# Kernel optimization log

Measured on AMD Instinct MI355X. Metric: run time of the kernel, lower is better.

Reference implementation:

```python
import jax, jax.numpy as jnp
import numpy as np
import math

B = 4096
D = 768
HID = 256
C_OLD = 100
C_NEW = 100
NUM_CLASSES = 200
EPSILON = 0.05
TAU = 0.1
EPS = 1e-8
NEG_INF = -1e9


def _l2_normalize(x):
    # matches F.normalize(p=2, dim=1, eps=1e-12)
    n = jnp.linalg.norm(x, axis=1, keepdims=True)
    return x / jnp.maximum(n, 1e-12)


def setup_inputs() -> dict:
    key = jax.random.key(0)
    k1, k2, k3, k4, k5, k6, k7 = jax.random.split(key, 7)
    z_u = jax.random.normal(k1, (B, D), dtype=jnp.float32)
    logits = jax.random.normal(k2, (B, NUM_CLASSES), dtype=jnp.float32)
    old_class_indices = jnp.arange(C_OLD, dtype=jnp.int64 if jax.config.jax_enable_x64 else jnp.int32)
    new_class_indices = jnp.arange(C_OLD, C_OLD + C_NEW, dtype=old_class_indices.dtype)
    base_features = jax.random.normal(k3, (B, D), dtype=jnp.float32)
    s = 1.0 / math.sqrt(D)
    f1_w = jax.random.uniform(k4, (HID, D), dtype=jnp.float32, minval=-s, maxval=s)
    f1_b = jax.random.uniform(k5, (HID,), dtype=jnp.float32, minval=-s, maxval=s)
    f2_w = jax.random.uniform(k6, (HID, D), dtype=jnp.float32, minval=-s, maxval=s)
    f2_b = jax.random.uniform(k7, (HID,), dtype=jnp.float32, minval=-s, maxval=s)
    return {"z_u": z_u, "logits": logits, "old_class_indices": old_class_indices,
            "new_class_indices": new_class_indices, "base_features": base_features,
            "f1_w": f1_w, "f1_b": f1_b, "f2_w": f2_w, "f2_b": f2_b}


def reference(z_u, logits, old_class_indices, new_class_indices, base_features,
              f1_w, f1_b, f2_w, f2_b):
    num_old = old_class_indices.shape[0]
    active = jnp.concatenate([old_class_indices, new_class_indices])

    # ---- soft entropy regularization ----
    probs = jax.nn.softmax(logits[:, active], axis=1)   # (B, C_old+C_new)
    mean_probs = probs.mean(axis=0)
    p_old = mean_probs[:num_old].sum()
    p_new = mean_probs[num_old:].sum()
    loss_inter = (p_old * jnp.log(p_old + EPS) + p_new * jnp.log(p_new + EPS)
                  + math.log(2.0))
    p_old_in = mean_probs[:num_old] / (p_old + EPS)
    loss_old_in = jnp.sum(p_old_in * jnp.log(p_old_in + EPS)) + math.log(num_old)
    p_new_in = mean_probs[num_old:] / (p_new + EPS)
    num_new = new_class_indices.shape[0]
    if num_new > 1:
        loss_new_in = jnp.sum(p_new_in * jnp.log(p_new_in + EPS)) + math.log(num_new)
    else:
        loss_new_in = jnp.float32(0.0)
    loss_entropy = loss_inter + loss_old_in + loss_new_in

    # ---- neighborhood mask from frozen base features ----
    base_norm = _l2_normalize(base_features)
    base_sim = base_norm @ base_norm.T                  # (B, B)
    eye = jnp.eye(base_sim.shape[0], dtype=bool)
    mask = (base_sim > EPSILON) & ~eye                  # (B, B) bool

    # ---- contrastive similarities ----
    z_norm = _l2_normalize(z_u)
    sim = z_norm @ z_norm.T                             # (B, B)

    f1_z = z_u @ f1_w.T + f1_b                          # (B, HID)
    f2_z = z_u @ f2_w.T + f2_b
    attn_logits = jnp.where(mask, f1_z @ f2_z.T, NEG_INF)
    w_ik = jax.nn.softmax(attn_logits, axis=1) * mask.astype(sim.dtype)

    exp_sim = jnp.where(eye, 0.0, jnp.exp(sim / TAU))
    denom = exp_sim.sum(axis=1, keepdims=True)
    log_prob = sim / TAU - jnp.log(denom + EPS)

    num_neighbors = mask.sum(axis=1).astype(sim.dtype)  # (B,)
    valid = num_neighbors > 0
    loss_i = -(w_ik * mask.astype(sim.dtype) * log_prob).sum(axis=1)
    per_sample = jnp.where(valid, loss_i / jnp.maximum(num_neighbors, 1.0), 0.0)
    n_valid = valid.sum().astype(sim.dtype)
    loss_contrastive = jnp.where(n_valid > 0,
                                 per_sample.sum() / jnp.maximum(n_valid, 1.0),
                                 0.0)

    total_loss = loss_entropy + loss_contrastive
    return total_loss
```

## Files before the change

### kernel.cpp

```cpp
#include <hip/hip_runtime.h>
#include <hip/hip_fp8.h>


#define B_N   4096
#define D_N   768
#define HID_N 256
#define NCLS  200
#define NJOBS 1056u

typedef __attribute__((ext_vector_type(8))) short v8s;
typedef __attribute__((ext_vector_type(4))) float v4f;

__device__ __forceinline__ unsigned char f2fp8(float x) {
    __hip_fp8_e4m3 v(x);
    return (unsigned char)v.__x;
}
__device__ __forceinline__ unsigned int pack4fp8(float a, float b, float c, float d) {
    return (unsigned int)f2fp8(a) | ((unsigned int)f2fp8(b) << 8) |
           ((unsigned int)f2fp8(c) << 16) | ((unsigned int)f2fp8(d) << 24);
}
__device__ __forceinline__ unsigned int pk2bf_trunc(float lo, float hi) {
    return (__float_as_uint(hi) & 0xFFFF0000u) | (__float_as_uint(lo) >> 16);
}

__device__ __forceinline__ void gld16c(const unsigned char* g, unsigned char* l) {
    __builtin_amdgcn_global_load_lds(
        (__attribute__((address_space(1))) void*)g,
        (__attribute__((address_space(3))) void*)l, 16, 0, 0);
}

#define ZERO_ACC24(a) { _Pragma("unroll") for (int _i = 0; _i < 2; _i++) \
    _Pragma("unroll") for (int _j = 0; _j < 4; _j++) a[_i][_j] = (v4f){0.f,0.f,0.f,0.f}; }

__global__ __launch_bounds__(256) void pre_all(
    const float* __restrict__ z, const float* __restrict__ base,
    const float* __restrict__ w1, const float* __restrict__ w2,
    const float* __restrict__ b1, const float* __restrict__ b2,
    const float* __restrict__ logits, const int* __restrict__ oldi,
    const int* __restrict__ newi,
    unsigned char* __restrict__ zn8, unsigned char* __restrict__ bn8,
    unsigned char* __restrict__ f1z8, unsigned char* __restrict__ f2z8,
    float* __restrict__ mpart, float* __restrict__ accums)
{
    __shared__ __align__(16) unsigned char shmem[2 * 64 * 72 * 2];
    int tid = threadIdx.x;

    if (blockIdx.x < 512) {
        unsigned short* Al = (unsigned short*)shmem;
        unsigned short* Bl = Al + 64 * 72;
        int f = blockIdx.x;
        int which = f >> 8;
        int t6 = f & 255;
        int mBase = (t6 >> 2) * 64;
        int nBase = (t6 & 3) * 64;
        const float* wsrc = which ? w2 : w1;
        const float* bias = which ? b2 : b1;
        unsigned char* outz = which ? f2z8 : f1z8;
        int lane = tid & 63, wave = tid >> 6, quad = lane >> 4, col = lane & 15;
        v4f acc[4];
        #pragma unroll
        for (int i = 0; i < 4; i++) acc[i] = (v4f){0.f, 0.f, 0.f, 0.f};
        for (int kc = 0; kc < D_N; kc += 64) {
            __syncthreads();
            #pragma unroll
            for (int s = 0; s < 4; s++) {
                int slot = s * 256 + tid;
                int row = slot >> 4, k4 = slot & 15;
                float4 va = *(const float4*)(z + (size_t)(mBase + row) * D_N + kc + k4 * 4);
                float4 vb = *(const float4*)(wsrc + (size_t)(nBase + row) * D_N + kc + k4 * 4);
                uint2 ua, ub;
                ua.x = pk2bf_trunc(va.x, va.y); ua.y = pk2bf_trunc(va.z, va.w);
                ub.x = pk2bf_trunc(vb.x, vb.y); ub.y = pk2bf_trunc(vb.z, vb.w);
                *(uint2*)(Al + row * 72 + k4 * 4) = ua;
                *(uint2*)(Bl + row * 72 + k4 * 4) = ub;
            }
            __syncthreads();
            #pragma unroll
            for (int kk = 0; kk < 2; kk++) {
                v8s af = *(const v8s*)(Al + (wave * 16 + col) * 72 + kk * 32 + quad * 8);
                #pragma unroll
                for (int tc = 0; tc < 4; tc++) {
                    v8s bf = *(const v8s*)(Bl + (tc * 16 + col) * 72 + kk * 32 + quad * 8);
                    acc[tc] = __builtin_amdgcn_mfma_f32_16x16x32_bf16(af, bf, acc[tc], 0, 0, 0);
                }
            }
        }
        #pragma unroll
        for (int tc = 0; tc < 4; tc++) {
            int gcol = nBase + tc * 16 + col;
            float bv = bias[gcol];
            #pragma unroll
            for (int reg = 0; reg < 4; reg++) {
                int grow = mBase + wave * 16 + quad * 4 + reg;
                int sw8 = ((grow >> 3) & 1) << 3;
                outz[(size_t)grow * HID_N + (gcol ^ sw8)] =
                    f2fp8(4.0f * (acc[tc][reg] + bv));
            }
        }
        return;
    }
    if (blockIdx.x < 768) {
        int* act = (int*)shmem;
        float* accs = (float*)(shmem + 1024);
        int sb = blockIdx.x - 512;
        int lane = tid & 63, wave = tid >> 6;
        if (sb == 0 && tid < 6) accums[tid] = 0.0f;
        if (tid < NCLS) act[tid] = (tid < 100) ? oldi[tid] : newi[tid - 100];
        accs[tid] = 0.f; accs[256 + tid] = 0.f; accs[512 + tid] = 0.f; accs[768 + tid] = 0.f;
        __syncthreads();
        int a0 = act[lane], a1 = act[lane + 64], a2 = act[lane + 128];
        int a3 = (lane < 8) ? act[lane + 192] : 0;
        int r0 = sb * 16 + wave * 4;
        float c0 = 0.f, c1 = 0.f, c2 = 0.f, c3 = 0.f;
        for (int i = 0; i < 4; i++) {
            const float* lr = logits + (size_t)(r0 + i) * NCLS;
            float x0 = lr[a0], x1 = lr[a1], x2 = lr[a2];
            float x3 = (lane < 8) ? lr[a3] : -3.0e38f;
            float m = fmaxf(fmaxf(x0, x1), fmaxf(x2, x3));
            #pragma unroll
            for (int s = 32; s > 0; s >>= 1) m = fmaxf(m, __shfl_xor(m, s));
            float e0 = __expf(x0 - m), e1 = __expf(x1 - m), e2 = __expf(x2 - m);
            float e3 = (lane < 8) ? __expf(x3 - m) : 0.f;
            float sm = e0 + e1 + e2 + e3;
            #pragma unroll
            for (int s = 32; s > 0; s >>= 1) sm += __shfl_xor(sm, s);
            float inv = 1.0f / sm;
            c0 += e0 * inv; c1 += e1 * inv; c2 += e2 * inv; c3 += e3 * inv;
        }
        accs[wave * 256 + lane] = c0; accs[wave * 256 + lane + 64] = c1;
        accs[wave * 256 + lane + 128] = c2;
        if (lane < 8) accs[wave * 256 + lane + 192] = c3;
        __syncthreads();
        mpart[(size_t)tid * 256 + sb] =
            accs[tid] + accs[256 + tid] + accs[512 + tid] + accs[768 + tid];
        return;
    }
    {
        int nb = blockIdx.x - 768;
        int lane = tid & 63, wave = tid >> 6;
        #pragma unroll
        for (int rr = 0; rr < 2; rr++) {
            int row = nb * 8 + rr * 4 + wave;
            const float* zr = z    + (size_t)row * D_N;
            const float* br = base + (size_t)row * D_N;
            float4 zv0 = *(const float4*)(zr + (size_t)lane * 4);
            float4 zv1 = *(const float4*)(zr + (size_t)(lane + 64) * 4);
            float4 zv2 = *(const float4*)(zr + (size_t)(lane + 128) * 4);
            float4 bv0 = *(const float4*)(br + (size_t)lane * 4);
            float4 bv1 = *(const float4*)(br + (size_t)(lane + 64) * 4);
            float4 bv2 = *(const float4*)(br + (size_t)(lane + 128) * 4);
            float s1 = zv0.x*zv0.x + zv0.y*zv0.y + zv0.z*zv0.z + zv0.w*zv0.w
                     + zv1.x*zv1.x + zv1.y*zv1.y + zv1.z*zv1.z + zv1.w*zv1.w
                     + zv2.x*zv2.x + zv2.y*zv2.y + zv2.z*zv2.z + zv2.w*zv2.w;
            float s2 = bv0.x*bv0.x + bv0.y*bv0.y + bv0.z*bv0.z + bv0.w*bv0.w
                     + bv1.x*bv1.x + bv1.y*bv1.y + bv1.z*bv1.z + bv1.w*bv1.w
                     + bv2.x*bv2.x + bv2.y*bv2.y + bv2.z*bv2.z + bv2.w*bv2.w;
            #pragma unroll
            for (int m = 32; m > 0; m >>= 1) {
                s1 += __shfl_xor(s1, m);
                s2 += __shfl_xor(s2, m);
            }
            float sc1 = 16.0f / fmaxf(sqrtf(s1), 1e-12f);
            float sc2 = 16.0f / fmaxf(sqrtf(s2), 1e-12f);
            size_t o = (size_t)row * D_N;
            int sw8 = ((row >> 3) & 1) << 3;
            *(unsigned int*)(zn8 + o + (((lane      ) * 4) ^ sw8)) =
                pack4fp8(zv0.x*sc1, zv0.y*sc1, zv0.z*sc1, zv0.w*sc1);
            *(unsigned int*)(zn8 + o + (((lane +  64) * 4) ^ sw8)) =
                pack4fp8(zv1.x*sc1, zv1.y*sc1, zv1.z*sc1, zv1.w*sc1);
            *(unsigned int*)(zn8 + o + (((lane + 128) * 4) ^ sw8)) =
                pack4fp8(zv2.x*sc1, zv2.y*sc1, zv2.z*sc1, zv2.w*sc1);
            *(unsigned int*)(bn8 + o + (((lane      ) * 4) ^ sw8)) =
                pack4fp8(bv0.x*sc2, bv0.y*sc2, bv0.z*sc2, bv0.w*sc2);
            *(unsigned int*)(bn8 + o + (((lane +  64) * 4) ^ sw8)) =
                pack4fp8(bv1.x*sc2, bv1.y*sc2, bv1.z*sc2, bv1.w*sc2);
            *(unsigned int*)(bn8 + o + (((lane + 128) * 4) ^ sw8)) =
                pack4fp8(bv2.x*sc2, bv2.y*sc2, bv2.z*sc2, bv2.w*sc2);
        }
    }
}

__global__ __launch_bounds__(256, 2) void main_fused(
    const unsigned char* __restrict__ zn8, const unsigned char* __restrict__ bn8,
    const unsigned char* __restrict__ f1z8, const unsigned char* __restrict__ f2z8,
    float* __restrict__ partials, int* __restrict__ jobcnt)
{
    __shared__ __align__(16) unsigned char S[53248];
    __shared__ int sh_j;
    unsigned char* SA_B = S;
    unsigned char* SA_S = S + 8192;
    unsigned char* SB_B = S + 16384;
    unsigned char* SB_S = S + 32768;
    unsigned char* F1   = S;
    unsigned char* F2   = S + 16384;
    float4* red = (float4*)(S + 49152);

    int tid = threadIdx.x, lane = tid & 63, wave = tid >> 6;
    int quad = lane >> 4, col = lane & 15;
    int wr3 = wave >> 1, wc3 = wave & 1;
    const int r8 = lane >> 3;
    const int kbl8 = (lane & 7) ^ r8;
    const int sub8 = ((quad & 1) ^ (col >> 3)) << 3;

    for (;;) {
        __syncthreads();
        if (tid == 0) sh_j = atomicAdd(jobcnt, 1);
        __syncthreads();
        unsigned int j = (unsigned int)sh_j;
        if (j >= NJOBS) return;

        int ib, jc, h; bool diag;
        if (j < 992u) {
            int pp = (int)(j >> 1); h = (int)(j & 1u); diag = false;
            int t = (int)((1.0f + sqrtf(8.0f * (float)pp + 1.0f)) * 0.5f);
            t = (t < 1) ? 1 : ((t > 31) ? 31 : t);
            while (t > 1  && t * (t - 1) / 2 > pp) --t;
            while (t < 31 && (t + 1) * t / 2 <= pp) ++t;
            jc = t; ib = pp - t * (t - 1) / 2;
        } else {
            int dd = (int)(j - 992u); ib = jc = dd >> 1; h = dd & 1; diag = true;
        }
        int aRow0 = ib * 128 + h * 64;
        int bRow0 = jc * 128;

        v4f accB[2][4], accS[2][4];
        ZERO_ACC24(accB); ZERO_ACC24(accS);
        for (int kc = 0; kc < D_N; kc += 128) {
            __syncthreads();
            #pragma unroll
            for (int s = 0; s < 4; s++) {
                int rowbase = s * 32 + wave * 8;
                size_t gOff = (size_t)(bRow0 + rowbase + r8) * D_N + kc + kbl8 * 16;
                gld16c(bn8 + gOff, SB_B + rowbase * 128);
                gld16c(zn8 + gOff, SB_S + rowbase * 128);
            }
            if (!diag) {
                #pragma unroll
                for (int s = 0; s < 2; s++) {
                    int rowbase = s * 32 + wave * 8;
                    size_t gOff = (size_t)(aRow0 + rowbase + r8) * D_N + kc + kbl8 * 16;
                    gld16c(bn8 + gOff, SA_B + rowbase * 128);
                    gld16c(zn8 + gOff, SA_S + rowbase * 128);
                }
            }
            __syncthreads();
            const unsigned char* AB = diag ? (SB_B + h * 64 * 128) : SA_B;
            const unsigned char* AS = diag ? (SB_S + h * 64 * 128) : SA_S;
            #pragma unroll
            for (int kk = 0; kk < 4; kk++) {
                int gbase = kk * 2 + (quad >> 1);
                int off = ((gbase ^ (col & 7)) << 4) + sub8;
                long a1[2], a2[2], b1[4], b2[4];
                #pragma unroll
                for (int t = 0; t < 2; t++) {
                    int rA = (wr3 * 32 + t * 16 + col) * 128;
                    a1[t] = *(const long*)(AB + rA + off);
                    a2[t] = *(const long*)(AS + rA + off);
                }
                #pragma unroll
                for (int t = 0; t < 4; t++) {
                    int rB = (wc3 * 64 + t * 16 + col) * 128;
                    b1[t] = *(const long*)(SB_B + rB + off);
                    b2[t] = *(const long*)(SB_S + rB + off);
                }
                #pragma unroll
                for (int tr = 0; tr < 2; tr++)
                    #pragma unroll
                    for (int tc = 0; tc < 4; tc++) {
                        accB[tr][tc] = __builtin_amdgcn_mfma_f32_16x16x32_fp8_fp8(
                            a1[tr], b1[tc], accB[tr][tc], 0, 0, 0);
                        accS[tr][tc] = __builtin_amdgcn_mfma_f32_16x16x32_fp8_fp8(
                            a2[tr], b2[tc], accS[tr][tc], 0, 0, 0);
                    }
            }
        }

        __syncthreads();
        {
            int r4 = lane >> 4;
            #pragma unroll
            for (int s = 0; s < 8; s++) {
                int rowbase = s * 16 + wave * 4;
                int row = rowbase + r4;
                int kb = (lane & 15) ^ (row & 15);
                gld16c(f2z8 + (size_t)(bRow0 + row) * HID_N + kb * 16, F2 + rowbase * 256);
            }
            #pragma unroll
            for (int s = 0; s < 4; s++) {
                int rowbase = s * 16 + wave * 4;
                int row = rowbase + r4;
                int kb = (lane & 15) ^ (row & 15);
                gld16c(f1z8 + (size_t)(aRow0 + row) * HID_N + kb * 16, F1 + rowbase * 256);
            }
        }

        unsigned int mb = 0u;
        #pragma unroll
        for (int tr = 0; tr < 2; tr++)
            #pragma unroll
            for (int tc = 0; tc < 4; tc++)
                #pragma unroll
                for (int reg = 0; reg < 4; reg++) {
                    int grow = aRow0 + wr3 * 32 + tr * 16 + quad * 4 + reg;
                    int gcol = bRow0 + wc3 * 64 + tc * 16 + col;
                    if (accB[tr][tc][reg] > 12.8f && grow != gcol)
                        mb |= 1u << (tr * 16 + tc * 4 + reg);
                }

        v4f accA[2][4]; ZERO_ACC24(accA);
        __syncthreads();
        #pragma unroll
        for (int kk = 0; kk < 8; kk++) {
            int gbase = kk * 2 + (quad >> 1);
            int off = ((gbase ^ col) << 4) + sub8;
            long af[2], bf[4];
            #pragma unroll
            for (int t = 0; t < 2; t++)
                af[t] = *(const long*)(F1 + (wr3 * 32 + t * 16 + col) * 256 + off);
            #pragma unroll
            for (int t = 0; t < 4; t++)
                bf[t] = *(const long*)(F2 + (wc3 * 64 + t * 16 + col) * 256 + off);
            #pragma unroll
            for (int tr = 0; tr < 2; tr++)
                #pragma unroll
                for (int tc = 0; tc < 4; tc++)
                    accA[tr][tc] = __builtin_amdgcn_mfma_f32_16x16x32_fp8_fp8(
                        af[tr], bf[tc], accA[tr][tc], 0, 0, 0);
        }

        __syncthreads();
        if (!diag) {
            int r4 = lane >> 4;
            #pragma unroll
            for (int s = 0; s < 8; s++) {
                int rowbase = s * 16 + wave * 4;
                int row = rowbase + r4;
                int kb = (lane & 15) ^ (row & 15);
                gld16c(f1z8 + (size_t)(bRow0 + row) * HID_N + kb * 16, F2 + rowbase * 256);
            }
            #pragma unroll
            for (int s = 0; s < 4; s++) {
                int rowbase = s * 16 + wave * 4;
                int row = rowbase + r4;
                int kb = (lane & 15) ^ (row & 15);
                gld16c(f2z8 + (size_t)(aRow0 + row) * HID_N + kb * 16, F1 + rowbase * 256);
            }
        }

        #pragma unroll
        for (int tr = 0; tr < 2; tr++) {
            float ls[4], as[4], nn[4], ds[4];
            #pragma unroll
            for (int r = 0; r < 4; r++) { ls[r]=0.f; as[r]=0.f; nn[r]=0.f; ds[r]=0.f; }
            #pragma unroll
            for (int tc = 0; tc < 4; tc++)
                #pragma unroll
                for (int reg = 0; reg < 4; reg++) {
                    float sv = accS[tr][tc][reg] * 0.00390625f;
                    int grow = aRow0 + wr3 * 32 + tr * 16 + quad * 4 + reg;
                    int gcol = bRow0 + wc3 * 64 + tc * 16 + col;
                    if (grow != gcol) ds[reg] += __expf(sv * 10.0f);
                    if ((mb >> (tr * 16 + tc * 4 + reg)) & 1u) {
                        float e = __expf(accA[tr][tc][reg] * 0.0625f);
                        ls[reg] += e; as[reg] += e * sv; nn[reg] += 1.f;
                    }
                }
            #pragma unroll
            for (int r = 0; r < 4; r++) {
                #pragma unroll
                for (int m = 1; m < 16; m <<= 1) {
                    ls[r] += __shfl_xor(ls[r], m);
                    as[r] += __shfl_xor(as[r], m);
                    ds[r] += __shfl_xor(ds[r], m);
                    nn[r] += __shfl_xor(nn[r], m);
                }
                if (col == 0) {
                    int row = aRow0 + wr3 * 32 + tr * 16 + quad * 4 + r;
                    float4 v; v.x = ls[r]; v.y = as[r]; v.z = ds[r]; v.w = nn[r];
                    *(float4*)(partials + ((size_t)row * 64 + jc * 2 + wc3) * 4) = v;
                }
            }
        }

        if (!diag) {
            ZERO_ACC24(accA);
            __syncthreads();
            #pragma unroll
            for (int kk = 0; kk < 8; kk++) {
                int gbase = kk * 2 + (quad >> 1);
                int off = ((gbase ^ col) << 4) + sub8;
                long af[2], bf[4];
                #pragma unroll
                for (int t = 0; t < 2; t++)
                    af[t] = *(const long*)(F1 + (wr3 * 32 + t * 16 + col) * 256 + off);
                #pragma unroll
                for (int t = 0; t < 4; t++)
                    bf[t] = *(const long*)(F2 + (wc3 * 64 + t * 16 + col) * 256 + off);
                #pragma unroll
                for (int tr = 0; tr < 2; tr++)
                    #pragma unroll
                    for (int tc = 0; tc < 4; tc++)
                        accA[tr][tc] = __builtin_amdgcn_mfma_f32_16x16x32_fp8_fp8(
                            af[tr], bf[tc], accA[tr][tc], 0, 0, 0);
            }
            #pragma unroll
            for (int tc = 0; tc < 4; tc++) {
                float l2 = 0.f, a2 = 0.f, d2 = 0.f, n2 = 0.f;
                #pragma unroll
                for (int tr = 0; tr < 2; tr++)
                    #pragma unroll
                    for (int reg = 0; reg < 4; reg++) {
                        float sv = accS[tr][tc][reg] * 0.00390625f;
                        d2 += __expf(sv * 10.0f);
                        if ((mb >> (tr * 16 + tc * 4 + reg)) & 1u) {
                            float e = __expf(accA[tr][tc][reg] * 0.0625f);
                            l2 += e; a2 += e * sv; n2 += 1.f;
                        }
                    }
                #pragma unroll
                for (int m = 16; m < 64; m <<= 1) {
                    l2 += __shfl_xor(l2, m);
                    a2 += __shfl_xor(a2, m);
                    d2 += __shfl_xor(d2, m);
                    n2 += __shfl_xor(n2, m);
                }
                if (lane < 16) {
                    float4 v; v.x = l2; v.y = a2; v.z = d2; v.w = n2;
                    red[wr3 * 128 + wc3 * 64 + tc * 16 + lane] = v;
                }
            }
            __syncthreads();
            if (tid < 128) {
                float4 u = red[tid], v = red[128 + tid];
                float4 w; w.x = u.x + v.x; w.y = u.y + v.y;
                w.z = u.z + v.z; w.w = u.w + v.w;
                *(float4*)(partials + ((size_t)(bRow0 + tid) * 64 + ib * 2 + h) * 4) = w;
            }
        }
    }
}

__global__ __launch_bounds__(256) void row_reduce_fin(
    const float* __restrict__ partials, const float* __restrict__ mpart,
    float* __restrict__ acc, float* __restrict__ out)
{
    int tid = threadIdx.x;
    int row = blockIdx.x * 64 + (tid >> 2);
    int sub = tid & 3;
    const float4* p = (const float4*)partials + (size_t)row * 64 + sub * 16;
    float L = 0.f, A = 0.f, Dn = 0.f, NN = 0.f;
    #pragma unroll
    for (int c = 0; c < 16; c++) { float4 v = p[c]; L += v.x; A += v.y; Dn += v.z; NN += v.w; }
    #pragma unroll
    for (int m = 1; m < 4; m <<= 1) {
        L += __shfl_xor(L, m); A += __shfl_xor(A, m);
        Dn += __shfl_xor(Dn, m); NN += __shfl_xor(NN, m);
    }
    float per = 0.f, val = 0.f;
    if (sub == 0 && NN > 0.5f) {
        per = (logf(Dn + 1e-8f) - 10.0f * (A / L)) / NN;
        val = 1.0f;
    }
    __shared__ float red[256];
    __shared__ float r2s[256];
    __shared__ int amLast;
    red[tid] = per; r2s[tid] = val; __syncthreads();
    for (int s = 128; s > 0; s >>= 1) {
        if (tid < s) { red[tid] += red[tid + s]; r2s[tid] += r2s[tid + s]; }
        __syncthreads();
    }
    if (tid == 0) {
        atomicAdd(&acc[0], red[0]);
        atomicAdd(&acc[1], r2s[0]);
        __threadfence();
        int old = atomicAdd((int*)&acc[2], 1);
        amLast = (old == (int)gridDim.x - 1);
    }
    __syncthreads();
    if (!amLast) return;

    __shared__ float bcast[2];
    float pcl = 0.0f;
    if (tid < NCLS) {
        const float4* mp = (const float4*)(mpart + (size_t)tid * 256);
        float s = 0.f;
        #pragma unroll
        for (int c = 0; c < 64; c++) { float4 v = mp[c]; s += v.x + v.y + v.z + v.w; }
        pcl = s * (1.0f / 4096.0f);
    }
    red[tid] = (tid < 100) ? pcl : 0.0f; __syncthreads();
    for (int s = 128; s > 0; s >>= 1) { if (tid < s) red[tid] += red[tid + s]; __syncthreads(); }
    if (tid == 0) bcast[0] = red[0];
    __syncthreads();
    red[tid] = (tid >= 100 && tid < NCLS) ? pcl : 0.0f; __syncthreads();
    for (int s = 128; s > 0; s >>= 1) { if (tid < s) red[tid] += red[tid + s]; __syncthreads(); }
    if (tid == 0) bcast[1] = red[0];
    __syncthreads();
    float p_old = bcast[0], p_new = bcast[1];

    float t = 0.0f;
    if (tid < 100)       { float q = pcl / (p_old + 1e-8f); t = q * logf(q + 1e-8f); }
    else if (tid < NCLS) { float q = pcl / (p_new + 1e-8f); t = q * logf(q + 1e-8f); }
    red[tid] = t; __syncthreads();
    for (int s = 128; s > 0; s >>= 1) { if (tid < s) red[tid] += red[tid + s]; __syncthreads(); }

    if (tid == 0) {
        float s0 = __hip_atomic_load(&acc[0], __ATOMIC_RELAXED, __HIP_MEMORY_SCOPE_AGENT);
        float s1 = __hip_atomic_load(&acc[1], __ATOMIC_RELAXED, __HIP_MEMORY_SCOPE_AGENT);
        float loss_inter = p_old * logf(p_old + 1e-8f) + p_new * logf(p_new + 1e-8f)
                           + 0.69314718056f;
        float loss_entropy = loss_inter + red[0] + 2.0f * 4.60517018599f;
        float lc = (s1 > 0.5f) ? s0 / s1 : 0.0f;
        out[0] = loss_entropy + lc;
    }
}

extern "C" void kernel_launch(void* const* d_in, const int* in_sizes, int n_in,
                              void* d_out, int out_size, void* d_ws, size_t ws_size,
                              hipStream_t stream)
{
    const float* z_u    = (const float*)d_in[0];
    const float* logits = (const float*)d_in[1];
    const int*   oldi   = (const int*)d_in[2];
    const int*   newi   = (const int*)d_in[3];
    const float* basef  = (const float*)d_in[4];
    const float* f1w    = (const float*)d_in[5];
    const float* f1b    = (const float*)d_in[6];
    const float* f2w    = (const float*)d_in[7];
    const float* f2b    = (const float*)d_in[8];
    float* out = (float*)d_out;

    unsigned char* zn8   = (unsigned char*)d_ws;
    unsigned char* bn8   = zn8 + (size_t)B_N * D_N;
    unsigned char* f1z8  = bn8 + (size_t)B_N * D_N;
    unsigned char* f2z8  = f1z8 + (size_t)B_N * HID_N;
    float* partials = (float*)(f2z8 + (size_t)B_N * HID_N);
    float* mpart    = partials + (size_t)B_N * 64 * 4;
    float* accums   = mpart + 256 * 256;
    int*   jobcnt   = (int*)(accums + 4);

    pre_all<<<512 + 256 + 512, 256, 0, stream>>>(
        z_u, basef, f1w, f2w, f1b, f2b, logits, oldi, newi,
        zn8, bn8, f1z8, f2z8, mpart, accums);
    main_fused<<<512, 256, 0, stream>>>(zn8, bn8, f1z8, f2z8, partials, jobcnt);
    row_reduce_fin<<<64, 256, 0, stream>>>(partials, mpart, accums, out);
}
```

Baseline: 165.0 us.

## Split projection GEMM into bf16 pre-conversion pass and async-LDS-load GEMM kernel

The fused preprocessing kernel no longer runs the f1/f2 projection GEMM with on-the-fly fp32-to-bf16 conversion. It now writes bf16 copies of z and the weight matrices to workspace. A new fz_gemm kernel then loads those with global_load_lds into XOR-swizzled shared memory and runs MFMA over larger K chunks. This removes redundant fp32 reads and per-tile conversion of z across the four column tiles, at the cost of an extra kernel launch, extra bf16 workspace traffic, and a serialization point between the passes.

```diff
diff --git a/kernel.cpp b/kernel.cpp
--- a/kernel.cpp
+++ b/kernel.cpp
@@ -32,112 +32,21 @@
 #define ZERO_ACC24(a) { _Pragma("unroll") for (int _i = 0; _i < 2; _i++) \
     _Pragma("unroll") for (int _j = 0; _j < 4; _j++) a[_i][_j] = (v4f){0.f,0.f,0.f,0.f}; }
 
-__global__ __launch_bounds__(256) void pre_all(
+__global__ __launch_bounds__(256) void pre0(
     const float* __restrict__ z, const float* __restrict__ base,
     const float* __restrict__ w1, const float* __restrict__ w2,
-    const float* __restrict__ b1, const float* __restrict__ b2,
     const float* __restrict__ logits, const int* __restrict__ oldi,
     const int* __restrict__ newi,
     unsigned char* __restrict__ zn8, unsigned char* __restrict__ bn8,
-    unsigned char* __restrict__ f1z8, unsigned char* __restrict__ f2z8,
+    unsigned short* __restrict__ zbf, unsigned short* __restrict__ wbf,
     float* __restrict__ mpart, float* __restrict__ accums)
 {
-    __shared__ __align__(16) unsigned char shmem[2 * 64 * 72 * 2];
+    __shared__ __align__(16) unsigned char shmem[8192];
     int tid = threadIdx.x;
+    int lane = tid & 63, wave = tid >> 6;
 
     if (blockIdx.x < 512) {
-        unsigned short* Al = (unsigned short*)shmem;
-        unsigned short* Bl = Al + 64 * 72;
-        int f = blockIdx.x;
-        int which = f >> 8;
-        int t6 = f & 255;
-        int mBase = (t6 >> 2) * 64;
-        int nBase = (t6 & 3) * 64;
-        const float* wsrc = which ? w2 : w1;
-        const float* bias = which ? b2 : b1;
-        unsigned char* outz = which ? f2z8 : f1z8;
-        int lane = tid & 63, wave = tid >> 6, quad = lane >> 4, col = lane & 15;
-        v4f acc[4];
-        #pragma unroll
-        for (int i = 0; i < 4; i++) acc[i] = (v4f){0.f, 0.f, 0.f, 0.f};
-        for (int kc = 0; kc < D_N; kc += 64) {
-            __syncthreads();
-            #pragma unroll
-            for (int s = 0; s < 4; s++) {
-                int slot = s * 256 + tid;
-                int row = slot >> 4, k4 = slot & 15;
-                float4 va = *(const float4*)(z + (size_t)(mBase + row) * D_N + kc + k4 * 4);
-                float4 vb = *(const float4*)(wsrc + (size_t)(nBase + row) * D_N + kc + k4 * 4);
-                uint2 ua, ub;
-                ua.x = pk2bf_trunc(va.x, va.y); ua.y = pk2bf_trunc(va.z, va.w);
-                ub.x = pk2bf_trunc(vb.x, vb.y); ub.y = pk2bf_trunc(vb.z, vb.w);
-                *(uint2*)(Al + row * 72 + k4 * 4) = ua;
-                *(uint2*)(Bl + row * 72 + k4 * 4) = ub;
-            }
-            __syncthreads();
-            #pragma unroll
-            for (int kk = 0; kk < 2; kk++) {
-                v8s af = *(const v8s*)(Al + (wave * 16 + col) * 72 + kk * 32 + quad * 8);
-                #pragma unroll
-                for (int tc = 0; tc < 4; tc++) {
-                    v8s bf = *(const v8s*)(Bl + (tc * 16 + col) * 72 + kk * 32 + quad * 8);
-                    acc[tc] = __builtin_amdgcn_mfma_f32_16x16x32_bf16(af, bf, acc[tc], 0, 0, 0);
-                }
-            }
-        }
-        #pragma unroll
-        for (int tc = 0; tc < 4; tc++) {
-            int gcol = nBase + tc * 16 + col;
-            float bv = bias[gcol];
-            #pragma unroll
-            for (int reg = 0; reg < 4; reg++) {
-                int grow = mBase + wave * 16 + quad * 4 + reg;
-                int sw8 = ((grow >> 3) & 1) << 3;
-                outz[(size_t)grow * HID_N + (gcol ^ sw8)] =
-                    f2fp8(4.0f * (acc[tc][reg] + bv));
-            }
-        }
-        return;
-    }
-    if (blockIdx.x < 768) {
-        int* act = (int*)shmem;
-        float* accs = (float*)(shmem + 1024);
-        int sb = blockIdx.x - 512;
-        int lane = tid & 63, wave = tid >> 6;
-        if (sb == 0 && tid < 6) accums[tid] = 0.0f;
-        if (tid < NCLS) act[tid] = (tid < 100) ? oldi[tid] : newi[tid - 100];
-        accs[tid] = 0.f; accs[256 + tid] = 0.f; accs[512 + tid] = 0.f; accs[768 + tid] = 0.f;
-        __syncthreads();
-        int a0 = act[lane], a1 = act[lane + 64], a2 = act[lane + 128];
-        int a3 = (lane < 8) ? act[lane + 192] : 0;
-        int r0 = sb * 16 + wave * 4;
-        float c0 = 0.f, c1 = 0.f, c2 = 0.f, c3 = 0.f;
-        for (int i = 0; i < 4; i++) {
-            const float* lr = logits + (size_t)(r0 + i) * NCLS;
-            float x0 = lr[a0], x1 = lr[a1], x2 = lr[a2];
-            float x3 = (lane < 8) ? lr[a3] : -3.0e38f;
-            float m = fmaxf(fmaxf(x0, x1), fmaxf(x2, x3));
-            #pragma unroll
-            for (int s = 32; s > 0; s >>= 1) m = fmaxf(m, __shfl_xor(m, s));
-            float e0 = __expf(x0 - m), e1 = __expf(x1 - m), e2 = __expf(x2 - m);
-            float e3 = (lane < 8) ? __expf(x3 - m) : 0.f;
-            float sm = e0 + e1 + e2 + e3;
-            #pragma unroll
-            for (int s = 32; s > 0; s >>= 1) sm += __shfl_xor(sm, s);
-            float inv = 1.0f / sm;
-            c0 += e0 * inv; c1 += e1 * inv; c2 += e2 * inv; c3 += e3 * inv;
-        }
-        accs[wave * 256 + lane] = c0; accs[wave * 256 + lane + 64] = c1;
-        accs[wave * 256 + lane + 128] = c2;
-        if (lane < 8) accs[wave * 256 + lane + 192] = c3;
-        __syncthreads();
-        mpart[(size_t)tid * 256 + sb] =
-            accs[tid] + accs[256 + tid] + accs[512 + tid] + accs[768 + tid];
-        return;
-    }
-    {
-        int nb = blockIdx.x - 768;
-        int lane = tid & 63, wave = tid >> 6;
+        int nb = blockIdx.x;
         #pragma unroll
         for (int rr = 0; rr < 2; rr++) {
             int row = nb * 8 + rr * 4 + wave;
@@ -149,6 +58,14 @@
             float4 bv0 = *(const float4*)(br + (size_t)lane * 4);
             float4 bv1 = *(const float4*)(br + (size_t)(lane + 64) * 4);
             float4 bv2 = *(const float4*)(br + (size_t)(lane + 128) * 4);
+            unsigned short* zbr = zbf + (size_t)row * D_N;
+            uint2 u0, u1, u2;
+            u0.x = pk2bf_trunc(zv0.x, zv0.y); u0.y = pk2bf_trunc(zv0.z, zv0.w);
+            u1.x = pk2bf_trunc(zv1.x, zv1.y); u1.y = pk2bf_trunc(zv1.z, zv1.w);
+            u2.x = pk2bf_trunc(zv2.x, zv2.y); u2.y = pk2bf_trunc(zv2.z, zv2.w);
+            *(uint2*)(zbr + lane * 4)       = u0;
+            *(uint2*)(zbr + lane * 4 + 256) = u1;
+            *(uint2*)(zbr + lane * 4 + 512) = u2;
             float s1 = zv0.x*zv0.x + zv0.y*zv0.y + zv0.z*zv0.z + zv0.w*zv0.w
                      + zv1.x*zv1.x + zv1.y*zv1.y + zv1.z*zv1.z + zv1.w*zv1.w
                      + zv2.x*zv2.x + zv2.y*zv2.y + zv2.z*zv2.z + zv2.w*zv2.w;
@@ -177,6 +94,125 @@
             *(unsigned int*)(bn8 + o + (((lane + 128) * 4) ^ sw8)) =
                 pack4fp8(bv2.x*sc2, bv2.y*sc2, bv2.z*sc2, bv2.w*sc2);
         }
+        return;
+    }
+    if (blockIdx.x < 768) {
+        int* act = (int*)shmem;
+        float* accs = (float*)(shmem + 1024);
+        int sb = blockIdx.x - 512;
+        if (sb == 0 && tid < 6) accums[tid] = 0.0f;
+        if (tid < NCLS) act[tid] = (tid < 100) ? oldi[tid] : newi[tid - 100];
+        accs[tid] = 0.f; accs[256 + tid] = 0.f; accs[512 + tid] = 0.f; accs[768 + tid] = 0.f;
+        __syncthreads();
+        int a0 = act[lane], a1 = act[lane + 64], a2 = act[lane + 128];
+        int a3 = (lane < 8) ? act[lane + 192] : 0;
+        int r0 = sb * 16 + wave * 4;
+        float c0 = 0.f, c1 = 0.f, c2 = 0.f, c3 = 0.f;
+        for (int i = 0; i < 4; i++) {
+            const float* lr = logits + (size_t)(r0 + i) * NCLS;
+            float x0 = lr[a0], x1 = lr[a1], x2 = lr[a2];
+            float x3 = (lane < 8) ? lr[a3] : -3.0e38f;
+            float m = fmaxf(fmaxf(x0, x1), fmaxf(x2, x3));
+            #pragma unroll
+            for (int s = 32; s > 0; s >>= 1) m = fmaxf(m, __shfl_xor(m, s));
+            float e0 = __expf(x0 - m), e1 = __expf(x1 - m), e2 = __expf(x2 - m);
+            float e3 = (lane < 8) ? __expf(x3 - m) : 0.f;
+            float sm = e0 + e1 + e2 + e3;
+            #pragma unroll
+            for (int s = 32; s > 0; s >>= 1) sm += __shfl_xor(sm, s);
+            float inv = 1.0f / sm;
+            c0 += e0 * inv; c1 += e1 * inv; c2 += e2 * inv; c3 += e3 * inv;
+        }
+        accs[wave * 256 + lane] = c0; accs[wave * 256 + lane + 64] = c1;
+        accs[wave * 256 + lane + 128] = c2;
+        if (lane < 8) accs[wave * 256 + lane + 192] = c3;
+        __syncthreads();
+        mpart[(size_t)tid * 256 + sb] =
+            accs[tid] + accs[256 + tid] + accs[512 + tid] + accs[768 + tid];
+        return;
+    }
+    {
+        int nb = blockIdx.x - 768;
+        #pragma unroll
+        for (int rr = 0; rr < 2; rr++) {
+            int r = nb * 8 + rr * 4 + wave;
+            const float* src = ((r >> 8) ? w2 : w1) + (size_t)(r & 255) * D_N;
+            unsigned short* dst = wbf + (size_t)r * D_N;
+            float4 v0 = *(const float4*)(src + (size_t)lane * 4);
+            float4 v1 = *(const float4*)(src + (size_t)(lane + 64) * 4);
+            float4 v2 = *(const float4*)(src + (size_t)(lane + 128) * 4);
+            uint2 u0, u1, u2;
+            u0.x = pk2bf_trunc(v0.x, v0.y); u0.y = pk2bf_trunc(v0.z, v0.w);
+            u1.x = pk2bf_trunc(v1.x, v1.y); u1.y = pk2bf_trunc(v1.z, v1.w);
+            u2.x = pk2bf_trunc(v2.x, v2.y); u2.y = pk2bf_trunc(v2.z, v2.w);
+            *(uint2*)(dst + lane * 4)       = u0;
+            *(uint2*)(dst + lane * 4 + 256) = u1;
+            *(uint2*)(dst + lane * 4 + 512) = u2;
+        }
+    }
+}
+
+__global__ __launch_bounds__(256) void fz_gemm(
+    const unsigned short* __restrict__ zbf, const unsigned short* __restrict__ wbf,
+    const float* __restrict__ b1, const float* __restrict__ b2,
+    unsigned char* __restrict__ f1z8, unsigned char* __restrict__ f2z8)
+{
+    __shared__ __align__(16) unsigned char S[2 * 64 * 256];
+    unsigned char* Al = S;
+    unsigned char* Bl = S + 64 * 256;
+
+    int tid = threadIdx.x, lane = tid & 63, wave = tid >> 6;
+    int quad = lane >> 4, col = lane & 15;
+    int f = blockIdx.x;
+    int which = f >> 8;
+    int t6 = f & 255;
+    int mBase = (t6 >> 2) * 64;
+    int nBase = (t6 & 3) * 64;
+    const float* bias = which ? b2 : b1;
+    unsigned char* outz = which ? f2z8 : f1z8;
+    const unsigned short* arow0 = zbf + (size_t)mBase * D_N;
+    const unsigned short* brow0 = wbf + (size_t)(which * 256 + nBase) * D_N;
+
+    int r4 = lane >> 4;
+    v4f acc[4];
+    #pragma unroll
+    for (int i = 0; i < 4; i++) acc[i] = (v4f){0.f, 0.f, 0.f, 0.f};
+
+    for (int kc = 0; kc < 6; kc++) {
+        __syncthreads();
+        #pragma unroll
+        for (int s = 0; s < 4; s++) {
+            int rowbase = s * 16 + wave * 4;
+            int row = rowbase + r4;
+            int kb = (lane & 15) ^ (row & 15);
+            gld16c((const unsigned char*)(arow0 + (size_t)row * D_N + kc * 128) + kb * 16,
+                   Al + rowbase * 256);
+            gld16c((const unsigned char*)(brow0 + (size_t)row * D_N + kc * 128) + kb * 16,
+                   Bl + rowbase * 256);
+        }
+        __syncthreads();
+        #pragma unroll
+        for (int kk = 0; kk < 4; kk++) {
+            int g = kk * 4 + quad;
+            v8s af = *(const v8s*)(Al + (wave * 16 + col) * 256 + ((g ^ col) << 4));
+            #pragma unroll
+            for (int tc = 0; tc < 4; tc++) {
+                v8s bf = *(const v8s*)(Bl + (tc * 16 + col) * 256 + ((g ^ col) << 4));
+                acc[tc] = __builtin_amdgcn_mfma_f32_16x16x32_bf16(af, bf, acc[tc], 0, 0, 0);
+            }
+        }
+    }
+    #pragma unroll
+    for (int tc = 0; tc < 4; tc++) {
+        int gcol = nBase + tc * 16 + col;
+        float bv = bias[gcol];
+        #pragma unroll
+        for (int reg = 0; reg < 4; reg++) {
+            int grow = mBase + wave * 16 + quad * 4 + reg;
+            int sw8 = ((grow >> 3) & 1) << 3;
+            outz[(size_t)grow * HID_N + (gcol ^ sw8)] =
+                f2fp8(4.0f * (acc[tc][reg] + bv));
+        }
     }
 }
 
@@ -538,10 +574,13 @@
     float* mpart    = partials + (size_t)B_N * 64 * 4;
     float* accums   = mpart + 256 * 256;
     int*   jobcnt   = (int*)(accums + 4);
-
-    pre_all<<<512 + 256 + 512, 256, 0, stream>>>(
-        z_u, basef, f1w, f2w, f1b, f2b, logits, oldi, newi,
-        zn8, bn8, f1z8, f2z8, mpart, accums);
+    unsigned short* zbf = (unsigned short*)(accums + 8);
+    unsigned short* wbf = zbf + (size_t)B_N * D_N;
+
+    pre0<<<512 + 256 + 64, 256, 0, stream>>>(
+        z_u, basef, f1w, f2w, logits, oldi, newi,
+        zn8, bn8, zbf, wbf, mpart, accums);
+    fz_gemm<<<512, 256, 0, stream>>>(zbf, wbf, f1b, f2b, f1z8, f2z8);
     main_fused<<<512, 256, 0, stream>>>(zn8, bn8, f1z8, f2z8, partials, jobcnt);
     row_reduce_fin<<<64, 256, 0, stream>>>(partials, mpart, accums, out);
 }
```

Result: no change. 168.0 us (+1.8%).
